# Kernel tuning notes

Hardware: AMD Instinct MI355X
Metric: run time of the kernel (lower is better)

Reference implementation:

```python
import jax, jax.numpy as jnp
import numpy as np

HEADS = 8
HIDDEN = 1536
HEAD_DIM = HIDDEN // HEADS
SCALE = HEAD_DIM ** -0.5


def setup_inputs() -> dict:
    key = jax.random.key(0)
    ks = jax.random.split(key, 10)
    B, S_IMG, S_TXT = 32, 1024, 77
    w = 0.02
    return {
        "img": jax.random.normal(ks[0], (B, S_IMG, HIDDEN), dtype=jnp.float32),
        "text": jax.random.normal(ks[1], (B, S_TXT, HIDDEN), dtype=jnp.float32),
        "Wq": jax.random.normal(ks[2], (HIDDEN, HIDDEN), dtype=jnp.float32) * w,
        "bq": jnp.zeros((HIDDEN,), dtype=jnp.float32),
        "Wk": jax.random.normal(ks[3], (HIDDEN, HIDDEN), dtype=jnp.float32) * w,
        "bk": jnp.zeros((HIDDEN,), dtype=jnp.float32),
        "Wv": jax.random.normal(ks[4], (HIDDEN, HIDDEN), dtype=jnp.float32) * w,
        "bv": jnp.zeros((HIDDEN,), dtype=jnp.float32),
        "Wo": jax.random.normal(ks[5], (HIDDEN, HIDDEN), dtype=jnp.float32) * w,
        "bo": jnp.zeros((HIDDEN,), dtype=jnp.float32),
    }


def reference(img, text, Wq, bq, Wk, bk, Wv, bv, Wo, bo):
    B, Sq, D = img.shape
    Sk = text.shape[1]
    # QKV projections (nn.Linear: y = x @ W.T + b)
    q = img @ Wq.T + bq    # [B, Sq, D]
    k = text @ Wk.T + bk   # [B, Sk, D]
    v = text @ Wv.T + bv
    # detach trick: position 0 of k/v has gradient stopped; forward value unchanged
    k0 = jax.lax.stop_gradient(k[:, :1, :])
    k = jnp.concatenate([k0, k[:, 1:, :]], axis=1)
    v0 = jax.lax.stop_gradient(v[:, :1, :])
    v = jnp.concatenate([v0, v[:, 1:, :]], axis=1)
    # split heads
    q = q.reshape(B, Sq, HEADS, HEAD_DIM)
    k = k.reshape(B, Sk, HEADS, HEAD_DIM)
    v = v.reshape(B, Sk, HEADS, HEAD_DIM)
    # attention scores and probs (mask is None in this module)
    scores = jnp.einsum("bqhd,bkhd->bhqk", q, k) * SCALE  # [B, H, Sq, Sk]
    probs = jax.nn.softmax(scores, axis=-1)
    out = jnp.einsum("bhqk,bkhd->bqhd", probs, v).reshape(B, Sq, D)
    return out @ Wo.T + bo
```

## Files before the change

kernel.cpp:

```cpp
#include <hip/hip_runtime.h>
#include <hip/hip_bf16.h>


typedef unsigned short u16;
typedef _Float16 f16x8 __attribute__((ext_vector_type(8)));
typedef __attribute__((ext_vector_type(8))) short s16x8;
typedef __attribute__((ext_vector_type(4))) float f32x4;
typedef __attribute__((ext_vector_type(4))) short s16x4;

#define MFMAH(a, b, c) __builtin_amdgcn_mfma_f32_16x16x32_f16(a, b, c, 0, 0, 0)

__device__ __forceinline__ u16 f2h(float x) {
    _Float16 h = (_Float16)x;
    return __builtin_bit_cast(u16, h);
}

__device__ __forceinline__ void gload16(const u16* g, const u16* l) {
    __builtin_amdgcn_global_load_lds(
        (const __attribute__((address_space(1))) unsigned int*)g,
        (__attribute__((address_space(3))) unsigned int*)l, 16, 0, 0);
}

__global__ void conv_h(const float* __restrict__ x, u16* __restrict__ h, int n8) {
    const int i = blockIdx.x * 256 + threadIdx.x;
    if (i >= n8) return;
    const f32x4 a = ((const f32x4*)x)[2 * i];
    const f32x4 b = ((const f32x4*)x)[2 * i + 1];
    u16 o[8];
#pragma unroll
    for (int j = 0; j < 4; ++j) { o[j] = f2h(a[j]); o[4 + j] = f2h(b[j]); }
    *(s16x8*)&h[(size_t)i << 3] = *(s16x8*)o;
}

struct Conv5Args {
    const float* x[5];
    u16* h[5];
    int n8[5];
};

__global__ void conv_h5(Conv5Args A) {
    const int z = blockIdx.y;
    const int i = blockIdx.x * 256 + threadIdx.x;
    if (i >= A.n8[z]) return;
    const float* x = A.x[z];
    const f32x4 a = ((const f32x4*)x)[2 * i];
    const f32x4 b = ((const f32x4*)x)[2 * i + 1];
    u16 o[8];
#pragma unroll
    for (int j = 0; j < 4; ++j) { o[j] = f2h(a[j]); o[4 + j] = f2h(b[j]); }
    *(s16x8*)&A.h[z][(size_t)i << 3] = *(s16x8*)o;
}

template <int OUTF32>
__global__ __launch_bounds__(512, 2) void gemm_h_nt(
    const u16* __restrict__ A,
    const u16* __restrict__ B0, const float* __restrict__ bias0, void* __restrict__ C0,
    const u16* __restrict__ B1, const float* __restrict__ bias1, void* __restrict__ C1,
    int M, int N, int K, int nby) {
    __shared__ u16 lds[32768];

    const u16* B = B0; const float* bias = bias0; void* Cout = C0;
    if (blockIdx.z) { B = B1; bias = bias1; Cout = C1; }

    const int nwg = gridDim.x;
    const int q8 = nwg >> 3, r8 = nwg & 7;
    const int xcd = blockIdx.x & 7, loc = blockIdx.x >> 3;
    const int wgid = (xcd < r8 ? xcd * (q8 + 1) : r8 * (q8 + 1) + (xcd - r8) * q8) + loc;
    const int bx = wgid / nby, by = wgid - bx * nby;
    const int row0 = bx * 256, col0 = by * 256;

    const int t = threadIdx.x, lane = t & 63, w = t >> 6;
    const int wr = w >> 2, wc = w & 3;
    const int l15 = lane & 15, lhi = lane >> 4;

    const u16* gA[2]; const u16* gB[2];
    const u16 *lA[2], *lB[2];
#pragma unroll
    for (int it = 0; it < 2; ++it) {
        const int ci = it * 512 + t;
        const int row = ci >> 2;
        const int g = (ci & 3) ^ ((row >> 1) & 3);
        int ar = row0 + row; if (ar > M - 1) ar = M - 1;
        gA[it] = A + (size_t)ar * K + (g << 3);
        gB[it] = B + (size_t)(col0 + row) * K + (g << 3);
        lA[it] = lds + ci * 8;
        lB[it] = lds + 8192 + ci * 8;
    }

    int aoff[8], boff[4];
#pragma unroll
    for (int mf = 0; mf < 8; ++mf) {
        const int ar = wr * 128 + mf * 16 + l15;
        aoff[mf] = ar * 32 + ((lhi ^ ((ar >> 1) & 3)) << 3);
    }
#pragma unroll
    for (int nf = 0; nf < 4; ++nf) {
        const int br = wc * 64 + nf * 16 + l15;
        boff[nf] = 8192 + br * 32 + ((lhi ^ ((br >> 1) & 3)) << 3);
    }

    f32x4 acc[8][4] = {};
    const int NT = K >> 5;

    gload16(gA[0], lA[0]); gload16(gA[1], lA[1]);
    gload16(gB[0], lB[0]); gload16(gB[1], lB[1]);

    for (int tt = 0; tt < NT; ++tt) {
        const int c = tt & 1;
        const int kn = ((tt + 1 < NT) ? tt + 1 : 0) << 5;
        const int sb = (c ^ 1) << 14;
        gload16(gA[0] + kn, lA[0] + sb); gload16(gA[1] + kn, lA[1] + sb);
        gload16(gB[0] + kn, lB[0] + sb); gload16(gB[1] + kn, lB[1] + sb);
        asm volatile("s_waitcnt vmcnt(4)" ::: "memory");
        __builtin_amdgcn_sched_barrier(0);
        __builtin_amdgcn_s_barrier();
        __builtin_amdgcn_sched_barrier(0);

        const int cb = c << 14;
        f16x8 a[8], b[4];
#pragma unroll
        for (int mf = 0; mf < 8; ++mf) a[mf] = *(const f16x8*)&lds[cb + aoff[mf]];
#pragma unroll
        for (int nf = 0; nf < 4; ++nf) b[nf] = *(const f16x8*)&lds[cb + boff[nf]];
        __builtin_amdgcn_s_setprio(1);
#pragma unroll
        for (int nf = 0; nf < 4; ++nf)
#pragma unroll
            for (int mf = 0; mf < 8; ++mf)
                acc[mf][nf] = MFMAH(a[mf], b[nf], acc[mf][nf]);
        __builtin_amdgcn_s_setprio(0);
        asm volatile("s_waitcnt lgkmcnt(0)" ::: "memory");
        __builtin_amdgcn_sched_barrier(0);
        __builtin_amdgcn_s_barrier();
        __builtin_amdgcn_sched_barrier(0);
    }
    asm volatile("s_waitcnt vmcnt(0)" ::: "memory");

#pragma unroll
    for (int nf = 0; nf < 4; ++nf) {
        const int col = col0 + wc * 64 + nf * 16 + l15;
        const float bs = bias[col];
#pragma unroll
        for (int mf = 0; mf < 8; ++mf) {
            const int row = row0 + wr * 128 + mf * 16 + (lhi << 2);
#pragma unroll
            for (int r = 0; r < 4; ++r) {
                if (row + r < M) {
                    const float v = acc[mf][nf][r] + bs;
                    if (OUTF32) ((float*)Cout)[(size_t)(row + r) * N + col] = v;
                    else        ((u16*)Cout)[(size_t)(row + r) * N + col] = f2h(v);
                }
            }
        }
    }
}

#define ALDK 200
#define ALDP 104

__global__ void attn_fused(const u16* __restrict__ qbuf, const u16* __restrict__ kbuf,
                           const u16* __restrict__ vbuf, u16* __restrict__ obuf) {
    __shared__ u16 Ks[80 * ALDK];
    __shared__ u16 Pls[64 * ALDP];
    __shared__ u16 Vt[96 * ALDP];

    const int t = threadIdx.x, lane = t & 63, w = t >> 6;
    const int qt = blockIdx.x, h = blockIdx.y, b = blockIdx.z;
    const int l15 = lane & 15, lhi = lane >> 4;

    f16x8 qf[6];
    {
        const size_t qrow = (size_t)(b * 1024 + qt * 64 + w * 16 + l15);
        const u16* qp = qbuf + qrow * 1536 + h * 192 + (lhi << 3);
#pragma unroll
        for (int kt = 0; kt < 6; ++kt) qf[kt] = *(const f16x8*)(qp + kt * 32);
    }

    for (int c = t; c < 80 * 24; c += 256) {
        const int s = c / 24, d8 = (c - s * 24) << 3;
        s16x8 val = {};
        if (s < 77) val = *(const s16x8*)&kbuf[(size_t)(b * 77 + s) * 1536 + h * 192 + d8];
        *(s16x8*)&Ks[s * ALDK + d8] = val;
    }
    for (int c = t; c < 96 * 12; c += 256) {
        const int s = c % 96, d8 = (c / 96) << 3;
        s16x8 val = {};
        if (s < 77) val = *(const s16x8*)&vbuf[(size_t)(b * 77 + s) * 1536 + h * 192 + d8];
#pragma unroll
        for (int j = 0; j < 8; ++j) Vt[(d8 + j) * ALDP + s] = (u16)val[j];
    }
    {
        const int row = w * 16 + l15;
        s16x4 z = {0, 0, 0, 0};
        *(s16x4*)&Pls[row * ALDP + 80 + (lhi << 2)] = z;
    }
    __syncthreads();

    f32x4 sacc[5] = {};
#pragma unroll
    for (int kt = 0; kt < 6; ++kt) {
#pragma unroll
        for (int nf = 0; nf < 5; ++nf) {
            f16x8 kf = *(const f16x8*)&Ks[(nf * 16 + l15) * ALDK + kt * 32 + (lhi << 3)];
            sacc[nf] = MFMAH(qf[kt], kf, sacc[nf]);
        }
    }

    float rps[4];
    const float scale = 0.07216878364870323f;
#pragma unroll
    for (int r = 0; r < 4; ++r) {
        float m = -1e30f;
#pragma unroll
        for (int nf = 0; nf < 5; ++nf) {
            const int c = nf * 16 + l15;
            const float sv = sacc[nf][r] * scale;
            if (c < 77) m = fmaxf(m, sv);
        }
#pragma unroll
        for (int off = 1; off < 16; off <<= 1) m = fmaxf(m, __shfl_xor(m, off));
        float sum = 0.f;
#pragma unroll
        for (int nf = 0; nf < 5; ++nf) {
            const int c = nf * 16 + l15;
            const float p = (c < 77) ? __expf(sacc[nf][r] * scale - m) : 0.f;
            sacc[nf][r] = p;
            sum += p;
        }
#pragma unroll
        for (int off = 1; off < 16; off <<= 1) sum += __shfl_xor(sum, off);
        rps[r] = 1.0f / sum;
    }

#pragma unroll
    for (int r = 0; r < 4; ++r)
#pragma unroll
        for (int nf = 0; nf < 5; ++nf)
            Pls[(w * 16 + (lhi << 2) + r) * ALDP + nf * 16 + l15] = f2h(sacc[nf][r]);
    __syncthreads();

    f16x8 pa[3];
#pragma unroll
    for (int kt = 0; kt < 3; ++kt)
        pa[kt] = *(const f16x8*)&Pls[(w * 16 + l15) * ALDP + kt * 32 + (lhi << 3)];

    const size_t orow = (size_t)(b * 1024 + qt * 64 + w * 16 + (lhi << 2));

    {
        f32x4 oacc[6] = {};
#pragma unroll
        for (int kt = 0; kt < 3; ++kt)
#pragma unroll
            for (int nf = 0; nf < 6; ++nf) {
                f16x8 vf = *(const f16x8*)&Vt[(nf * 16 + l15) * ALDP + kt * 32 + (lhi << 3)];
                oacc[nf] = MFMAH(pa[kt], vf, oacc[nf]);
            }
#pragma unroll
        for (int nf = 0; nf < 6; ++nf) {
            const int col = h * 192 + nf * 16 + l15;
#pragma unroll
            for (int r = 0; r < 4; ++r)
                obuf[(orow + r) * 1536 + col] = f2h(oacc[nf][r] * rps[r]);
        }
    }
    __syncthreads();
    for (int c = t; c < 96 * 12; c += 256) {
        const int s = c % 96, d8 = (c / 96) << 3;
        s16x8 val = {};
        if (s < 77) val = *(const s16x8*)&vbuf[(size_t)(b * 77 + s) * 1536 + h * 192 + 96 + d8];
#pragma unroll
        for (int j = 0; j < 8; ++j) Vt[(d8 + j) * ALDP + s] = (u16)val[j];
    }
    __syncthreads();
    {
        f32x4 oacc[6] = {};
#pragma unroll
        for (int kt = 0; kt < 3; ++kt)
#pragma unroll
            for (int nf = 0; nf < 6; ++nf) {
                f16x8 vf = *(const f16x8*)&Vt[(nf * 16 + l15) * ALDP + kt * 32 + (lhi << 3)];
                oacc[nf] = MFMAH(pa[kt], vf, oacc[nf]);
            }
#pragma unroll
        for (int nf = 0; nf < 6; ++nf) {
            const int col = h * 192 + 96 + nf * 16 + l15;
#pragma unroll
            for (int r = 0; r < 4; ++r)
                obuf[(orow + r) * 1536 + col] = f2h(oacc[nf][r] * rps[r]);
        }
    }
}

extern "C" void kernel_launch(void* const* d_in, const int* in_sizes, int n_in,
                              void* d_out, int out_size, void* d_ws, size_t ws_size,
                              hipStream_t stream) {
    const float* img  = (const float*)d_in[0];
    const float* text = (const float*)d_in[1];
    const float* Wq   = (const float*)d_in[2];
    const float* bq   = (const float*)d_in[3];
    const float* Wk   = (const float*)d_in[4];
    const float* bk   = (const float*)d_in[5];
    const float* Wv   = (const float*)d_in[6];
    const float* bv   = (const float*)d_in[7];
    const float* Wo   = (const float*)d_in[8];
    const float* bo   = (const float*)d_in[9];

    const size_t imgN = (size_t)32768 * 1536;
    const size_t txtN = (size_t)2464 * 1536;
    const size_t wN   = (size_t)1536 * 1536;

    u16* img_h = (u16*)d_ws;
    u16* qb    = img_h + imgN;
    u16* txt_h = qb + imgN;
    u16* Wq_h  = txt_h + txtN;
    u16* Wk_h  = Wq_h + wN;
    u16* Wv_h  = Wk_h + wN;
    u16* Wo_h  = Wv_h + wN;
    u16* kb    = Wo_h + wN;
    u16* vb    = kb + txtN;

    hipLaunchKernelGGL(conv_h, dim3((unsigned)(imgN / 8 / 256)), dim3(256),
                       0, stream, img, img_h, (int)(imgN / 8));
    Conv5Args ca;
    ca.x[0] = text; ca.h[0] = txt_h; ca.n8[0] = (int)(txtN / 8);
    ca.x[1] = Wq;   ca.h[1] = Wq_h;  ca.n8[1] = (int)(wN / 8);
    ca.x[2] = Wk;   ca.h[2] = Wk_h;  ca.n8[2] = (int)(wN / 8);
    ca.x[3] = Wv;   ca.h[3] = Wv_h;  ca.n8[3] = (int)(wN / 8);
    ca.x[4] = Wo;   ca.h[4] = Wo_h;  ca.n8[4] = (int)(wN / 8);
    hipLaunchKernelGGL(conv_h5, dim3((unsigned)((txtN / 8 + 255) / 256), 5),
                       dim3(256), 0, stream, ca);

    hipLaunchKernelGGL((gemm_h_nt<0>), dim3(768), dim3(512), 0, stream,
                       img_h, Wq_h, bq, (void*)qb, Wq_h, bq, (void*)qb,
                       32768, 1536, 1536, 6);
    hipLaunchKernelGGL((gemm_h_nt<0>), dim3(60, 1, 2), dim3(512), 0, stream,
                       txt_h, Wk_h, bk, (void*)kb, Wv_h, bv, (void*)vb,
                       2464, 1536, 1536, 6);
    hipLaunchKernelGGL(attn_fused, dim3(16, 8, 32), dim3(256), 0, stream,
                       qb, kb, vb, qb);
    hipLaunchKernelGGL((gemm_h_nt<1>), dim3(768), dim3(512), 0, stream,
                       qb, Wo_h, bo, d_out, Wo_h, bo, d_out,
                       32768, 1536, 1536, 6);
}
```

Baseline: 623.5 us.

## Deepen GEMM K-tile to 64 with staged loads interleaved across four MFMA phases

The fp16 NT GEMM now uses a 64-wide K tile (double-buffered, 128KB LDS) with an 8-way XOR swizzle. Each iteration is split into four quarter-phases, and global-to-LDS loads for the next tile are issued one quarter at a time between the MFMA batches. This halves the number of outer iterations and spreads memory traffic over the compute. In exchange it adds many more barriers per iteration, and the doubled LDS footprint may cut occupancy below the two blocks per CU requested by launch bounds.

```diff
diff --git a/kernel.cpp b/kernel.cpp
--- a/kernel.cpp
+++ b/kernel.cpp
@@ -57,7 +57,7 @@
     const u16* __restrict__ B0, const float* __restrict__ bias0, void* __restrict__ C0,
     const u16* __restrict__ B1, const float* __restrict__ bias1, void* __restrict__ C1,
     int M, int N, int K, int nby) {
-    __shared__ u16 lds[32768];
+    __shared__ u16 lds[65536];
 
     const u16* B = B0; const float* bias = bias0; void* Cout = C0;
     if (blockIdx.z) { B = B1; bias = bias1; Cout = C1; }
@@ -73,66 +73,100 @@
     const int wr = w >> 2, wc = w & 3;
     const int l15 = lane & 15, lhi = lane >> 4;
 
-    const u16* gA[2]; const u16* gB[2];
-    const u16 *lA[2], *lB[2];
-#pragma unroll
-    for (int it = 0; it < 2; ++it) {
-        const int ci = it * 512 + t;
-        const int row = ci >> 2;
-        const int g = (ci & 3) ^ ((row >> 1) & 3);
-        int ar = row0 + row; if (ar > M - 1) ar = M - 1;
-        gA[it] = A + (size_t)ar * K + (g << 3);
-        gB[it] = B + (size_t)(col0 + row) * K + (g << 3);
-        lA[it] = lds + ci * 8;
-        lB[it] = lds + 8192 + ci * 8;
-    }
-
-    int aoff[8], boff[4];
-#pragma unroll
-    for (int mf = 0; mf < 8; ++mf) {
-        const int ar = wr * 128 + mf * 16 + l15;
-        aoff[mf] = ar * 32 + ((lhi ^ ((ar >> 1) & 3)) << 3);
-    }
-#pragma unroll
-    for (int nf = 0; nf < 4; ++nf) {
-        const int br = wc * 64 + nf * 16 + l15;
-        boff[nf] = 8192 + br * 32 + ((lhi ^ ((br >> 1) & 3)) << 3);
+    const u16* gp[4][2];
+    int lof[4][2];
+#pragma unroll
+    for (int p = 0; p < 4; ++p)
+#pragma unroll
+        for (int it = 0; it < 2; ++it) {
+            const int ci = it * 512 + t;
+            const int rih = ci >> 3, slot = ci & 7;
+            const int gs = slot ^ (rih & 7);
+            if (p < 2) {
+                int gr = row0 + p * 128 + rih;
+                if (gr > M - 1) gr = M - 1;
+                gp[p][it] = A + (size_t)gr * K + (gs << 3);
+                lof[p][it] = p * 8192 + ci * 8;
+            } else {
+                const int gr = col0 + (p - 2) * 128 + rih;
+                gp[p][it] = B + (size_t)gr * K + (gs << 3);
+                lof[p][it] = 16384 + (p - 2) * 8192 + ci * 8;
+            }
+        }
+
+    int aof[8], bof[4];
+#pragma unroll
+    for (int i = 0; i < 8; ++i) {
+        const int ar = wr * 128 + i * 16 + l15;
+        aof[i] = ar * 64 + ((lhi ^ (ar & 7)) << 3);
+    }
+#pragma unroll
+    for (int n = 0; n < 4; ++n) {
+        const int br = wc * 64 + n * 16 + l15;
+        bof[n] = 16384 + br * 64 + ((lhi ^ (br & 7)) << 3);
     }
 
     f32x4 acc[8][4] = {};
-    const int NT = K >> 5;
-
-    gload16(gA[0], lA[0]); gload16(gA[1], lA[1]);
-    gload16(gB[0], lB[0]); gload16(gB[1], lB[1]);
+    const int NT = K >> 6;
+
+#pragma unroll
+    for (int p = 0; p < 4; ++p) {
+        gload16(gp[p][0], lds + lof[p][0]);
+        gload16(gp[p][1], lds + lof[p][1]);
+    }
+
+#define STAGE(p) do { gload16(gp[p][0] + kn, lsb + lof[p][0]); \
+                      gload16(gp[p][1] + kn, lsb + lof[p][1]); } while (0)
+#define BARX() do { __builtin_amdgcn_sched_barrier(0); __builtin_amdgcn_s_barrier(); \
+                    __builtin_amdgcn_sched_barrier(0); } while (0)
+#define LGKM0() do { asm volatile("s_waitcnt lgkmcnt(0)" ::: "memory"); \
+                     __builtin_amdgcn_sched_barrier(0); } while (0)
+#define MFMA_Q(mh) do { __builtin_amdgcn_s_setprio(1); \
+    _Pragma("unroll") for (int nf = 0; nf < 4; ++nf) \
+    _Pragma("unroll") for (int mf = 0; mf < 4; ++mf) \
+        acc[(mh) * 4 + mf][nf] = MFMAH(a[mf], bb[nf], acc[(mh) * 4 + mf][nf]); \
+    __builtin_amdgcn_s_setprio(0); } while (0)
 
     for (int tt = 0; tt < NT; ++tt) {
-        const int c = tt & 1;
-        const int kn = ((tt + 1 < NT) ? tt + 1 : 0) << 5;
-        const int sb = (c ^ 1) << 14;
-        gload16(gA[0] + kn, lA[0] + sb); gload16(gA[1] + kn, lA[1] + sb);
-        gload16(gB[0] + kn, lB[0] + sb); gload16(gB[1] + kn, lB[1] + sb);
-        asm volatile("s_waitcnt vmcnt(4)" ::: "memory");
-        __builtin_amdgcn_sched_barrier(0);
-        __builtin_amdgcn_s_barrier();
-        __builtin_amdgcn_sched_barrier(0);
-
-        const int cb = c << 14;
-        f16x8 a[8], b[4];
-#pragma unroll
-        for (int mf = 0; mf < 8; ++mf) a[mf] = *(const f16x8*)&lds[cb + aoff[mf]];
-#pragma unroll
-        for (int nf = 0; nf < 4; ++nf) b[nf] = *(const f16x8*)&lds[cb + boff[nf]];
-        __builtin_amdgcn_s_setprio(1);
-#pragma unroll
-        for (int nf = 0; nf < 4; ++nf)
-#pragma unroll
-            for (int mf = 0; mf < 8; ++mf)
-                acc[mf][nf] = MFMAH(a[mf], b[nf], acc[mf][nf]);
-        __builtin_amdgcn_s_setprio(0);
-        asm volatile("s_waitcnt lgkmcnt(0)" ::: "memory");
-        __builtin_amdgcn_sched_barrier(0);
-        __builtin_amdgcn_s_barrier();
-        __builtin_amdgcn_sched_barrier(0);
+        const int cb = (tt & 1) << 15;
+        u16* lsb = lds + (((tt & 1) ^ 1) << 15);
+        const size_t kn = (size_t)((tt + 1 < NT) ? tt + 1 : 0) << 6;
+
+        f16x8 a[4], bb[4];
+
+        STAGE(0);
+        asm volatile("s_waitcnt vmcnt(2)" ::: "memory");
+        BARX();
+#pragma unroll
+        for (int nf = 0; nf < 4; ++nf) bb[nf] = *(const f16x8*)&lds[cb + bof[nf]];
+#pragma unroll
+        for (int mf = 0; mf < 4; ++mf) a[mf] = *(const f16x8*)&lds[cb + aof[mf]];
+        LGKM0();
+        MFMA_Q(0);
+        BARX();
+#pragma unroll
+        for (int mf = 0; mf < 4; ++mf) a[mf] = *(const f16x8*)&lds[cb + aof[4 + mf]];
+        STAGE(1);
+        BARX();
+        LGKM0();
+        MFMA_Q(1);
+        BARX();
+#pragma unroll
+        for (int nf = 0; nf < 4; ++nf) bb[nf] = *(const f16x8*)&lds[cb + (bof[nf] ^ 32)];
+#pragma unroll
+        for (int mf = 0; mf < 4; ++mf) a[mf] = *(const f16x8*)&lds[cb + (aof[mf] ^ 32)];
+        STAGE(2);
+        BARX();
+        LGKM0();
+        MFMA_Q(0);
+        BARX();
+#pragma unroll
+        for (int mf = 0; mf < 4; ++mf) a[mf] = *(const f16x8*)&lds[cb + (aof[4 + mf] ^ 32)];
+        STAGE(3);
+        BARX();
+        LGKM0();
+        MFMA_Q(1);
+        BARX();
     }
     asm volatile("s_waitcnt vmcnt(0)" ::: "memory");
 
@@ -153,6 +187,10 @@
             }
         }
     }
+#undef STAGE
+#undef BARX
+#undef LGKM0
+#undef MFMA_Q
 }
 
 #define ALDK 200
```

Result: faster. 587.8 us (-5.7%).

## Deepen GEMM LDS pipeline to four stages with split MFMA and new swizzle

Applied to the files above, without the earlier changes.

The fp16 NT GEMM moves from a two-buffer LDS scheme to a four-slot ring with three K-tiles prefetched, and drops to one barrier per iteration instead of two. LDS reads for the A fragments are split into two halves so the first half of the MFMAs can start while the second half loads, and global loads are issued between the halves. The LDS swizzle changes to a different XOR of row bits to cut bank conflicts. LDS use doubles to 128 KB per block, which may cut the number of resident blocks below the launch_bounds target of two per CU.

```diff
diff --git a/kernel.cpp b/kernel.cpp
--- a/kernel.cpp
+++ b/kernel.cpp
@@ -20,6 +20,8 @@
         (const __attribute__((address_space(1))) unsigned int*)g,
         (__attribute__((address_space(3))) unsigned int*)l, 16, 0, 0);
 }
+
+__device__ __forceinline__ int rh(int r) { return (r & 3) ^ ((r >> 2) & 3); }
 
 __global__ void conv_h(const float* __restrict__ x, u16* __restrict__ h, int n8) {
     const int i = blockIdx.x * 256 + threadIdx.x;
@@ -57,7 +59,7 @@
     const u16* __restrict__ B0, const float* __restrict__ bias0, void* __restrict__ C0,
     const u16* __restrict__ B1, const float* __restrict__ bias1, void* __restrict__ C1,
     int M, int N, int K, int nby) {
-    __shared__ u16 lds[32768];
+    __shared__ u16 lds[65536];
 
     const u16* B = B0; const float* bias = bias0; void* Cout = C0;
     if (blockIdx.z) { B = B1; bias = bias1; Cout = C1; }
@@ -73,66 +75,89 @@
     const int wr = w >> 2, wc = w & 3;
     const int l15 = lane & 15, lhi = lane >> 4;
 
-    const u16* gA[2]; const u16* gB[2];
-    const u16 *lA[2], *lB[2];
+    const u16* gpA[2]; const u16* gpB[2];
+    int lofA[2], lofB[2];
 #pragma unroll
     for (int it = 0; it < 2; ++it) {
         const int ci = it * 512 + t;
-        const int row = ci >> 2;
-        const int g = (ci & 3) ^ ((row >> 1) & 3);
+        const int row = ci >> 2, slot = ci & 3;
+        const int gs = slot ^ rh(row);
         int ar = row0 + row; if (ar > M - 1) ar = M - 1;
-        gA[it] = A + (size_t)ar * K + (g << 3);
-        gB[it] = B + (size_t)(col0 + row) * K + (g << 3);
-        lA[it] = lds + ci * 8;
-        lB[it] = lds + 8192 + ci * 8;
-    }
-
-    int aoff[8], boff[4];
-#pragma unroll
-    for (int mf = 0; mf < 8; ++mf) {
-        const int ar = wr * 128 + mf * 16 + l15;
-        aoff[mf] = ar * 32 + ((lhi ^ ((ar >> 1) & 3)) << 3);
-    }
-#pragma unroll
-    for (int nf = 0; nf < 4; ++nf) {
-        const int br = wc * 64 + nf * 16 + l15;
-        boff[nf] = 8192 + br * 32 + ((lhi ^ ((br >> 1) & 3)) << 3);
+        gpA[it] = A + (size_t)ar * K + (gs << 3);
+        gpB[it] = B + (size_t)(col0 + row) * K + (gs << 3);
+        lofA[it] = ci * 8;
+        lofB[it] = 8192 + ci * 8;
+    }
+
+    const int ss = rh(l15);
+    int aof[8], bof[4];
+#pragma unroll
+    for (int i = 0; i < 8; ++i) {
+        const int ar = wr * 128 + i * 16 + l15;
+        aof[i] = ar * 32 + ((lhi ^ ss) << 3);
+    }
+#pragma unroll
+    for (int n = 0; n < 4; ++n) {
+        const int br = wc * 64 + n * 16 + l15;
+        bof[n] = 8192 + br * 32 + ((lhi ^ ss) << 3);
     }
 
     f32x4 acc[8][4] = {};
     const int NT = K >> 5;
 
-    gload16(gA[0], lA[0]); gload16(gA[1], lA[1]);
-    gload16(gB[0], lB[0]); gload16(gB[1], lB[1]);
+#define SBAR0() __builtin_amdgcn_sched_barrier(0)
+
+#pragma unroll
+    for (int p = 0; p < 3; ++p) {
+        const size_t kp = (size_t)p << 5;
+        u16* lb = lds + (p << 14);
+        gload16(gpA[0] + kp, lb + lofA[0]); gload16(gpA[1] + kp, lb + lofA[1]);
+        gload16(gpB[0] + kp, lb + lofB[0]); gload16(gpB[1] + kp, lb + lofB[1]);
+    }
+    asm volatile("s_waitcnt vmcnt(8)" ::: "memory");
+    SBAR0(); __builtin_amdgcn_s_barrier(); SBAR0();
 
     for (int tt = 0; tt < NT; ++tt) {
-        const int c = tt & 1;
-        const int kn = ((tt + 1 < NT) ? tt + 1 : 0) << 5;
-        const int sb = (c ^ 1) << 14;
-        gload16(gA[0] + kn, lA[0] + sb); gload16(gA[1] + kn, lA[1] + sb);
-        gload16(gB[0] + kn, lB[0] + sb); gload16(gB[1] + kn, lB[1] + sb);
-        asm volatile("s_waitcnt vmcnt(4)" ::: "memory");
-        __builtin_amdgcn_sched_barrier(0);
-        __builtin_amdgcn_s_barrier();
-        __builtin_amdgcn_sched_barrier(0);
-
-        const int cb = c << 14;
-        f16x8 a[8], b[4];
-#pragma unroll
-        for (int mf = 0; mf < 8; ++mf) a[mf] = *(const f16x8*)&lds[cb + aoff[mf]];
-#pragma unroll
-        for (int nf = 0; nf < 4; ++nf) b[nf] = *(const f16x8*)&lds[cb + boff[nf]];
+        const int cb = (tt & 3) << 14;
+        u16* lsb = lds + (((tt + 3) & 3) << 14);
+        const int tx = (tt + 3 < NT) ? tt + 3 : tt + 3 - NT;
+        const size_t kn = (size_t)tx << 5;
+
+        f16x8 a0[4], a1[4], bb[4];
+
+#pragma unroll
+        for (int nf = 0; nf < 4; ++nf) bb[nf] = *(const f16x8*)&lds[cb + bof[nf]];
+#pragma unroll
+        for (int mf = 0; mf < 4; ++mf) a0[mf] = *(const f16x8*)&lds[cb + aof[mf]];
+        SBAR0();
+#pragma unroll
+        for (int mf = 0; mf < 4; ++mf) a1[mf] = *(const f16x8*)&lds[cb + aof[4 + mf]];
+        gload16(gpA[0] + kn, lsb + lofA[0]);
+        gload16(gpA[1] + kn, lsb + lofA[1]);
+        gload16(gpB[0] + kn, lsb + lofB[0]);
+        gload16(gpB[1] + kn, lsb + lofB[1]);
+
+        asm volatile("s_waitcnt lgkmcnt(4)" ::: "memory");
+        SBAR0();
         __builtin_amdgcn_s_setprio(1);
 #pragma unroll
         for (int nf = 0; nf < 4; ++nf)
 #pragma unroll
-            for (int mf = 0; mf < 8; ++mf)
-                acc[mf][nf] = MFMAH(a[mf], b[nf], acc[mf][nf]);
+            for (int mf = 0; mf < 4; ++mf)
+                acc[mf][nf] = MFMAH(a0[mf], bb[nf], acc[mf][nf]);
         __builtin_amdgcn_s_setprio(0);
         asm volatile("s_waitcnt lgkmcnt(0)" ::: "memory");
-        __builtin_amdgcn_sched_barrier(0);
-        __builtin_amdgcn_s_barrier();
-        __builtin_amdgcn_sched_barrier(0);
+        SBAR0();
+        __builtin_amdgcn_s_setprio(1);
+#pragma unroll
+        for (int nf = 0; nf < 4; ++nf)
+#pragma unroll
+            for (int mf = 0; mf < 4; ++mf)
+                acc[4 + mf][nf] = MFMAH(a1[mf], bb[nf], acc[4 + mf][nf]);
+        __builtin_amdgcn_s_setprio(0);
+
+        asm volatile("s_waitcnt vmcnt(8)" ::: "memory");
+        SBAR0(); __builtin_amdgcn_s_barrier(); SBAR0();
     }
     asm volatile("s_waitcnt vmcnt(0)" ::: "memory");
 
@@ -153,6 +178,7 @@
             }
         }
     }
+#undef SBAR0
 }
 
 #define ALDK 200
```

After: 616.9 us. No clear change (-1.1%).
